# Optimization experiments

Hardware: AMD Instinct MI355X
Metric: run time of the kernel (lower is better)

## Reference

```python
import jax, jax.numpy as jnp
import numpy as np

N = 100000      # nodes
E = 3200000     # edges (before self-loops)
IN = 1          # input feature dim
H1, C = 4, 8    # layer1: 4 heads x 8 channels; layer2: 1 head x 8 channels
NEG_SLOPE = 0.2


def setup_inputs() -> dict:
    key = jax.random.key(0)
    ks = jax.random.split(key, 10)
    x = jax.random.normal(ks[0], (N, IN), jnp.float32)
    edge_index = jax.random.randint(ks[1], (2, E), 0, N, dtype=jnp.int32)
    # layer 1 params (GATConv(1, 8, heads=4))
    W1 = jax.random.normal(ks[2], (IN, H1 * C), jnp.float32) * 0.5
    a_src1 = jax.random.normal(ks[3], (H1, C), jnp.float32) * 0.5
    a_dst1 = jax.random.normal(ks[4], (H1, C), jnp.float32) * 0.5
    b1 = jnp.zeros((H1 * C,), jnp.float32)
    # layer 2 params (GATConv(32, 8, heads=1))
    W2 = jax.random.normal(ks[5], (H1 * C, C), jnp.float32) * 0.2
    a_src2 = jax.random.normal(ks[6], (1, C), jnp.float32) * 0.5
    a_dst2 = jax.random.normal(ks[7], (1, C), jnp.float32) * 0.5
    b2 = jnp.zeros((C,), jnp.float32)
    return {"x": x, "edge_index": edge_index, "W1": W1, "a_src1": a_src1,
            "a_dst1": a_dst1, "b1": b1, "W2": W2, "a_src2": a_src2,
            "a_dst2": a_dst2, "b2": b2}


def _gat_layer(x, src, dst, W, a_s, a_d, b, heads, ch):
    # Linear transform per head: [N, heads, ch]
    h = (x @ W).reshape(-1, heads, ch)
    # per-node attention logits
    al_s = jnp.einsum('nhc,hc->nh', h, a_s)  # [N, H]
    al_d = jnp.einsum('nhc,hc->nh', h, a_d)  # [N, H]
    # per-edge logits (message src -> dst)
    e = jax.nn.leaky_relu(al_s[src] + al_d[dst], NEG_SLOPE)  # [E', H]
    # segment softmax over incoming edges of each dst node
    m = jax.ops.segment_max(e, dst, num_segments=N)          # [N, H]
    e = jnp.exp(e - m[dst])
    s = jax.ops.segment_sum(e, dst, num_segments=N)          # [N, H]
    alpha = e / s[dst]                                       # [E', H]
    # weighted scatter-add aggregation
    out = jax.ops.segment_sum(h[src] * alpha[:, :, None], dst, num_segments=N)
    return out.reshape(N, heads * ch) + b


def reference(x, edge_index, W1, a_src1, a_dst1, b1, W2, a_src2, a_dst2, b2):
    loops = jnp.arange(N, dtype=edge_index.dtype)
    src = jnp.concatenate([edge_index[0], loops])  # add self-loops (PyG default)
    dst = jnp.concatenate([edge_index[1], loops])
    h = _gat_layer(x, src, dst, W1, a_src1, a_dst1, b1, H1, C)
    h = jax.nn.relu(h)
    out = _gat_layer(h, src, dst, W2, a_src2, a_dst2, b2, 1, C)
    return out
```

## Files before the change

kernel.cpp:

```cpp
#include <hip/hip_runtime.h>
#include <hip/hip_bf16.h>

#define NEG_SLOPE 0.2f


__global__ void prep_consts(const float* __restrict__ W1,
                            const float* __restrict__ as1,
                            const float* __restrict__ ad1,
                            float* __restrict__ consts) {
    int t = threadIdx.x;
    if (t >= 8) return;
    int h = t & 3;
    const float* a = (t < 4) ? as1 : ad1;
    float s = 0.f;
    #pragma unroll
    for (int c = 0; c < 8; ++c)
        s += W1[h * 8 + c] * a[h * 8 + c];
    consts[t] = s;
}

__global__ void bucket_hist(const int* __restrict__ ei, int* __restrict__ gcnt, int E) {
    __shared__ int cnt[2048];
    int t = threadIdx.x;
    for (int i = t; i < 2048; i += 256) cnt[i] = 0;
    __syncthreads();
    int stride = gridDim.x * 256;
    for (int e = blockIdx.x * 256 + t; e < E; e += stride)
        atomicAdd(&cnt[ei[E + e] >> 6], 1);
    __syncthreads();
    for (int i = t; i < 2048; i += 256) {
        int c = cnt[i];
        if (c) atomicAdd(&gcnt[i], c);
    }
}

__global__ void scan_init(const int* __restrict__ gcnt,
                          int* __restrict__ gbase, int* __restrict__ gcursor) {
    __shared__ int buf[512];
    int t = threadIdx.x;
    int c0 = gcnt[t * 4], c1 = gcnt[t * 4 + 1], c2 = gcnt[t * 4 + 2], c3 = gcnt[t * 4 + 3];
    int sum = c0 + c1 + c2 + c3;
    buf[t] = sum;
    __syncthreads();
    for (int o = 1; o < 512; o <<= 1) {
        int add = (t >= o) ? buf[t - o] : 0;
        __syncthreads();
        buf[t] += add;
        __syncthreads();
    }
    int base = buf[t] - sum;
    gbase[t * 4] = base;     gcursor[t * 4] = base;     base += c0;
    gbase[t * 4 + 1] = base; gcursor[t * 4 + 1] = base; base += c1;
    gbase[t * 4 + 2] = base; gcursor[t * 4 + 2] = base; base += c2;
    gbase[t * 4 + 3] = base; gcursor[t * 4 + 3] = base;
}

__global__ void bucket_scatter(const int* __restrict__ ei, int* __restrict__ gcursor,
                               unsigned int* __restrict__ pairs, int E) {
    __shared__ int cnt[2048];
    __shared__ int basel[2048];
    int t = threadIdx.x;
    int chunk = (E + gridDim.x - 1) / gridDim.x;
    int lo = blockIdx.x * chunk;
    int hi = min(E, lo + chunk);
    for (int i = t; i < 2048; i += 1024) cnt[i] = 0;
    __syncthreads();
    for (int e = lo + t; e < hi; e += 1024)
        atomicAdd(&cnt[ei[E + e] >> 6], 1);
    __syncthreads();
    for (int i = t; i < 2048; i += 1024) {
        int c = cnt[i];
        basel[i] = c ? atomicAdd(&gcursor[i], c) : 0;
        cnt[i] = 0;
    }
    __syncthreads();
    for (int e = lo + t; e < hi; e += 1024) {
        int s = ei[e];
        int d = ei[E + e];
        int bk = d >> 6;
        int loc = atomicAdd(&cnt[bk], 1);
        pairs[basel[bk] + loc] = (unsigned)s | ((unsigned)(d & 63) << 17);
    }
}

__global__ void l1_comb(const float* __restrict__ x,
                        const int* __restrict__ gbase, const int* __restrict__ gcnt,
                        const unsigned int* __restrict__ pairs,
                        const float* __restrict__ consts,
                        const float* __restrict__ W1, const float* __restrict__ b1,
                        const float* __restrict__ W2,
                        const float* __restrict__ as2, const float* __restrict__ ad2,
                        float* __restrict__ h2, float* __restrict__ als2,
                        float* __restrict__ ald2, int N) {
    __shared__ __align__(16) float R[4 * 64 * 8];
    __shared__ float xl[64];
    int t = threadIdx.x;
    int lane = t & 63;
    int bk = blockIdx.x;
    int node0 = bk << 6;
    int nw = min(64, N - node0);
    for (int i = t; i < 4 * 64 * 8; i += 256) R[i] = 0.f;
    if (t < nw) xl[t] = x[node0 + t];
    float S[4], D[4];
    #pragma unroll
    for (int h = 0; h < 4; ++h) { S[h] = consts[h]; D[h] = consts[4 + h]; }
    __syncthreads();
    float* wreg = &R[(t >> 6) * 512];
    int b = gbase[bk];
    int hi = b + gcnt[bk];
    for (int i = b + t; i < hi; i += 256) {
        unsigned p = pairs[i];
        int src = (int)(p & 131071u);
        int ld  = (int)(p >> 17);
        float xs = x[src];
        float xd = xl[ld];
        float w[4];
        #pragma unroll
        for (int h = 0; h < 4; ++h) {
            float v = xs * S[h] + xd * D[h];
            v = (v > 0.f) ? v : NEG_SLOPE * v;
            w[h] = __expf(v);
        }
        unsigned long long mask = ~0ull;
        #pragma unroll
        for (int bit = 0; bit < 6; ++bit) {
            unsigned long long bb = __ballot((ld >> bit) & 1);
            mask &= ((ld >> bit) & 1) ? bb : ~bb;
        }
        mask &= __ballot(1);
        int rank = __popcll(mask & ((1ull << lane) - 1ull));
        float* row = &wreg[ld * 8];
        for (int r = 0; r < 64; ++r) {
            if (__ballot(rank == r) == 0ull) break;
            if (rank == r) {
                row[0] += w[0]; row[1] += w[1]; row[2] += w[2]; row[3] += w[3];
                row[4] = fmaf(w[0], xs, row[4]); row[5] = fmaf(w[1], xs, row[5]);
                row[6] = fmaf(w[2], xs, row[6]); row[7] = fmaf(w[3], xs, row[7]);
            }
        }
    }
    __syncthreads();
    if (t < nw) {
        int n = node0 + t;
        float xn = xl[t];
        float o[8];
        #pragma unroll
        for (int c = 0; c < 8; ++c) o[c] = 0.f;
        #pragma unroll
        for (int h = 0; h < 4; ++h) {
            float v = xn * (S[h] + D[h]);
            v = (v > 0.f) ? v : NEG_SLOPE * v;
            float ww = __expf(v);
            float s1 = R[t * 8 + h] + R[512 + t * 8 + h]
                     + R[1024 + t * 8 + h] + R[1536 + t * 8 + h] + ww;
            float t1 = R[t * 8 + 4 + h] + R[512 + t * 8 + 4 + h]
                     + R[1024 + t * 8 + 4 + h] + R[1536 + t * 8 + 4 + h] + ww * xn;
            float tt = t1 / s1;
            #pragma unroll
            for (int c = 0; c < 8; ++c) {
                float r = fmaxf(tt * W1[h * 8 + c] + b1[h * 8 + c], 0.f);
                #pragma unroll
                for (int c2 = 0; c2 < 8; ++c2) o[c2] += r * W2[(h * 8 + c) * 8 + c2];
            }
        }
        float as = 0.f, ad = 0.f;
        #pragma unroll
        for (int c = 0; c < 8; ++c) { as += o[c] * as2[c]; ad += o[c] * ad2[c]; }
        float4* hv = (float4*)&h2[(size_t)n * 8];
        hv[0] = make_float4(o[0], o[1], o[2], o[3]);
        hv[1] = make_float4(o[4], o[5], o[6], o[7]);
        als2[n] = as;
        ald2[n] = ad;
    }
}

__global__ void l2_comb(const int* __restrict__ gbase, const int* __restrict__ gcnt,
                        const unsigned int* __restrict__ pairs,
                        const float* __restrict__ als2, const float* __restrict__ ald2,
                        const float* __restrict__ h2, const float* __restrict__ b2,
                        float* __restrict__ out, int N) {
    __shared__ __align__(16) float R[4 * 64 * 12];
    __shared__ float adl[64];
    int t = threadIdx.x;
    int lane = t & 63;
    int bk = blockIdx.x;
    int node0 = bk << 6;
    int nw = min(64, N - node0);
    for (int i = t; i < 4 * 64 * 12; i += 256) R[i] = 0.f;
    if (t < nw) adl[t] = ald2[node0 + t];
    __syncthreads();
    float* wreg = &R[(t >> 6) * 768];
    int b = gbase[bk];
    int hi = b + gcnt[bk];
    for (int i = b + t; i < hi; i += 256) {
        unsigned p = pairs[i];
        int src = (int)(p & 131071u);
        int ld  = (int)(p >> 17);
        float a = als2[src];
        const float4* hv = (const float4*)&h2[(size_t)src * 8];
        float4 ha = hv[0], hb = hv[1];
        float v = a + adl[ld];
        v = (v > 0.f) ? v : NEG_SLOPE * v;
        float w = __expf(v);
        unsigned long long mask = ~0ull;
        #pragma unroll
        for (int bit = 0; bit < 6; ++bit) {
            unsigned long long bb = __ballot((ld >> bit) & 1);
            mask &= ((ld >> bit) & 1) ? bb : ~bb;
        }
        mask &= __ballot(1);
        int rank = __popcll(mask & ((1ull << lane) - 1ull));
        float* row = &wreg[ld * 12];
        for (int r = 0; r < 64; ++r) {
            if (__ballot(rank == r) == 0ull) break;
            if (rank == r) {
                row[0] += w;
                row[1] = fmaf(w, ha.x, row[1]); row[2] = fmaf(w, ha.y, row[2]);
                row[3] = fmaf(w, ha.z, row[3]); row[4] = fmaf(w, ha.w, row[4]);
                row[5] = fmaf(w, hb.x, row[5]); row[6] = fmaf(w, hb.y, row[6]);
                row[7] = fmaf(w, hb.z, row[7]); row[8] = fmaf(w, hb.w, row[8]);
            }
        }
    }
    __syncthreads();
    if (t < nw) {
        int n = node0 + t;
        float v = als2[n] + adl[t];
        v = (v > 0.f) ? v : NEG_SLOPE * v;
        float ww = __expf(v);
        const float4* hv = (const float4*)&h2[(size_t)n * 8];
        float4 ha0 = hv[0], hb0 = hv[1];
        float acc[9];
        #pragma unroll
        for (int c = 0; c < 9; ++c)
            acc[c] = R[t * 12 + c] + R[768 + t * 12 + c]
                   + R[1536 + t * 12 + c] + R[2304 + t * 12 + c];
        float s2 = acc[0] + ww;
        float inv = 1.f / s2;
        float4* ov = (float4*)&out[(size_t)n * 8];
        ov[0] = make_float4((acc[1] + ww * ha0.x) * inv + b2[0],
                            (acc[2] + ww * ha0.y) * inv + b2[1],
                            (acc[3] + ww * ha0.z) * inv + b2[2],
                            (acc[4] + ww * ha0.w) * inv + b2[3]);
        ov[1] = make_float4((acc[5] + ww * hb0.x) * inv + b2[4],
                            (acc[6] + ww * hb0.y) * inv + b2[5],
                            (acc[7] + ww * hb0.z) * inv + b2[6],
                            (acc[8] + ww * hb0.w) * inv + b2[7]);
    }
}


__global__ void edge_pass1(const int* __restrict__ ei, const float* __restrict__ x,
                           const float* __restrict__ consts,
                           float* __restrict__ s1, float* __restrict__ t1, int E, int N) {
    int e = blockIdx.x * blockDim.x + threadIdx.x;
    if (e >= E + N) return;
    int src, dst;
    if (e < E) { src = ei[e]; dst = ei[E + e]; }
    else       { src = dst = e - E; }
    float xs = x[src], xd = x[dst];
    #pragma unroll
    for (int h = 0; h < 4; ++h) {
        float v = xs * consts[h] + xd * consts[4 + h];
        v = (v > 0.f) ? v : NEG_SLOPE * v;
        float w = __expf(v);
        atomicAdd(&s1[dst * 4 + h], w);
        atomicAdd(&t1[dst * 4 + h], w * xs);
    }
}

__global__ void node_mid(const float* __restrict__ s1, const float* __restrict__ t1,
                         const float* __restrict__ W1, const float* __restrict__ b1,
                         const float* __restrict__ W2,
                         const float* __restrict__ as2, const float* __restrict__ ad2,
                         float* __restrict__ h2, float* __restrict__ als2,
                         float* __restrict__ ald2, int N) {
    int n = blockIdx.x * blockDim.x + threadIdx.x;
    if (n >= N) return;
    float o[8];
    #pragma unroll
    for (int c = 0; c < 8; ++c) o[c] = 0.f;
    #pragma unroll
    for (int h = 0; h < 4; ++h) {
        float t = t1[n * 4 + h] / s1[n * 4 + h];
        #pragma unroll
        for (int c = 0; c < 8; ++c) {
            float r = fmaxf(t * W1[h * 8 + c] + b1[h * 8 + c], 0.f);
            #pragma unroll
            for (int c2 = 0; c2 < 8; ++c2) o[c2] += r * W2[(h * 8 + c) * 8 + c2];
        }
    }
    float as = 0.f, ad = 0.f;
    #pragma unroll
    for (int c = 0; c < 8; ++c) { h2[n * 8 + c] = o[c]; as += o[c] * as2[c]; ad += o[c] * ad2[c]; }
    als2[n] = as; ald2[n] = ad;
}

__global__ void edge_pass2(const int* __restrict__ ei, const float* __restrict__ als2,
                           const float* __restrict__ ald2, const float* __restrict__ h2,
                           float* __restrict__ s2, float* __restrict__ acc2, int E, int N) {
    int e = blockIdx.x * blockDim.x + threadIdx.x;
    if (e >= E + N) return;
    int src, dst;
    if (e < E) { src = ei[e]; dst = ei[E + e]; }
    else       { src = dst = e - E; }
    float v = als2[src] + ald2[dst];
    v = (v > 0.f) ? v : NEG_SLOPE * v;
    float w = __expf(v);
    atomicAdd(&s2[dst], w);
    const float4* hs = (const float4*)&h2[src * 8];
    float4 a = hs[0], bq = hs[1];
    float* acc = &acc2[dst * 8];
    atomicAdd(&acc[0], w * a.x);  atomicAdd(&acc[1], w * a.y);
    atomicAdd(&acc[2], w * a.z);  atomicAdd(&acc[3], w * a.w);
    atomicAdd(&acc[4], w * bq.x); atomicAdd(&acc[5], w * bq.y);
    atomicAdd(&acc[6], w * bq.z); atomicAdd(&acc[7], w * bq.w);
}

__global__ void node_out(const float* __restrict__ s2, const float* __restrict__ acc2,
                         const float* __restrict__ b2, float* __restrict__ out, int N) {
    int i = blockIdx.x * blockDim.x + threadIdx.x;
    if (i >= N * 8) return;
    out[i] = acc2[i] / s2[i >> 3] + b2[i & 7];
}


extern "C" void kernel_launch(void* const* d_in, const int* in_sizes, int n_in,
                              void* d_out, int out_size, void* d_ws, size_t ws_size,
                              hipStream_t stream) {
    const float* x   = (const float*)d_in[0];
    const int*   ei  = (const int*)d_in[1];
    const float* W1  = (const float*)d_in[2];
    const float* as1 = (const float*)d_in[3];
    const float* ad1 = (const float*)d_in[4];
    const float* b1  = (const float*)d_in[5];
    const float* W2  = (const float*)d_in[6];
    const float* as2 = (const float*)d_in[7];
    const float* ad2 = (const float*)d_in[8];
    const float* b2  = (const float*)d_in[9];
    float* out = (float*)d_out;

    const int N = in_sizes[0];
    const int E = in_sizes[1] / 2;
    const int NBK = (N + 63) >> 6;

    float* ws = (float*)d_ws;
    size_t need = (size_t)(16 + 3 * 2048 + 10 * (size_t)N + (size_t)E) * sizeof(float);

    if (N <= 131072 && ws_size >= need) {
        float*    consts  = ws;
        int*      gcnt    = (int*)(ws + 16);
        int*      gbase   = gcnt + 2048;
        int*      gcursor = gbase + 2048;
        float*    als2    = ws + 16 + 3 * 2048;
        float*    ald2    = als2 + N;
        float*    h2      = ald2 + N;
        unsigned* pairs   = (unsigned*)(h2 + 8 * (size_t)N);

        hipMemsetAsync(gcnt, 0, 2048 * sizeof(int), stream);
        prep_consts<<<1, 64, 0, stream>>>(W1, as1, ad1, consts);
        bucket_hist<<<128, 256, 0, stream>>>(ei, gcnt, E);
        scan_init<<<1, 512, 0, stream>>>(gcnt, gbase, gcursor);
        bucket_scatter<<<256, 1024, 0, stream>>>(ei, gcursor, pairs, E);
        l1_comb<<<NBK, 256, 0, stream>>>(x, gbase, gcnt, pairs, consts,
                                         W1, b1, W2, as2, ad2, h2, als2, ald2, N);
        l2_comb<<<NBK, 256, 0, stream>>>(gbase, gcnt, pairs, als2, ald2, h2, b2, out, N);
    } else {
        float* consts = ws;
        float* s1   = ws + 16;
        float* t1   = s1 + 4 * (size_t)N;
        float* h2   = t1 + 4 * (size_t)N;
        float* als2 = h2 + 8 * (size_t)N;
        float* ald2 = als2 + (size_t)N;
        float* s2   = ald2 + (size_t)N;
        float* acc2 = s2 + (size_t)N;

        hipMemsetAsync(ws, 0, (16 + 8 * (size_t)N) * sizeof(float), stream);
        hipMemsetAsync(s2, 0, 9 * (size_t)N * sizeof(float), stream);
        prep_consts<<<1, 64, 0, stream>>>(W1, as1, ad1, consts);
        int total = E + N;
        edge_pass1<<<(total + 255) / 256, 256, 0, stream>>>(ei, x, consts, s1, t1, E, N);
        node_mid<<<(N + 255) / 256, 256, 0, stream>>>(s1, t1, W1, b1, W2, as2, ad2, h2, als2, ald2, N);
        edge_pass2<<<(total + 255) / 256, 256, 0, stream>>>(ei, als2, ald2, h2, s2, acc2, E, N);
        node_out<<<(N * 8 + 255) / 256, 256, 0, stream>>>(s2, acc2, b2, out, N);
    }
}
```

Measured before the change: 223.8 us.

## Vectorize edge-index loads, fuse const prep, widen comb kernels with prefetch

Bucket histogram and scatter kernels now read destination and source indices as int4 vectors, with scalar head and tail loops for unaligned ends. The per-head constant computation is folded into the scan kernel, removing one launch. The l1/l2 combine kernels move from 256 to 512 threads with eight shared-memory partial-sum regions, and software-prefetch the next packed edge. The intent is to cut load instruction count and launch overhead and raise memory-level parallelism, at the cost of doubled shared memory per block and more reduction work in the epilogue.

```diff
diff --git a/kernel.cpp b/kernel.cpp
--- a/kernel.cpp
+++ b/kernel.cpp
@@ -4,29 +4,28 @@
 #define NEG_SLOPE 0.2f
 
 
-__global__ void prep_consts(const float* __restrict__ W1,
-                            const float* __restrict__ as1,
-                            const float* __restrict__ ad1,
-                            float* __restrict__ consts) {
-    int t = threadIdx.x;
-    if (t >= 8) return;
-    int h = t & 3;
-    const float* a = (t < 4) ? as1 : ad1;
-    float s = 0.f;
-    #pragma unroll
-    for (int c = 0; c < 8; ++c)
-        s += W1[h * 8 + c] * a[h * 8 + c];
-    consts[t] = s;
-}
-
 __global__ void bucket_hist(const int* __restrict__ ei, int* __restrict__ gcnt, int E) {
     __shared__ int cnt[2048];
     int t = threadIdx.x;
     for (int i = t; i < 2048; i += 256) cnt[i] = 0;
     __syncthreads();
-    int stride = gridDim.x * 256;
-    for (int e = blockIdx.x * 256 + t; e < E; e += stride)
-        atomicAdd(&cnt[ei[E + e] >> 6], 1);
+    const int* dei = ei + E;
+    int gid = blockIdx.x * 256 + t;
+    int gstride = gridDim.x * 256;
+    if ((E & 3) == 0) {
+        const int4* dei4 = (const int4*)dei;
+        int E4 = E >> 2;
+        for (int v = gid; v < E4; v += gstride) {
+            int4 d = dei4[v];
+            atomicAdd(&cnt[d.x >> 6], 1);
+            atomicAdd(&cnt[d.y >> 6], 1);
+            atomicAdd(&cnt[d.z >> 6], 1);
+            atomicAdd(&cnt[d.w >> 6], 1);
+        }
+    } else {
+        for (int e = gid; e < E; e += gstride)
+            atomicAdd(&cnt[dei[e] >> 6], 1);
+    }
     __syncthreads();
     for (int i = t; i < 2048; i += 256) {
         int c = cnt[i];
@@ -35,9 +34,22 @@
 }
 
 __global__ void scan_init(const int* __restrict__ gcnt,
-                          int* __restrict__ gbase, int* __restrict__ gcursor) {
+                          int* __restrict__ gbase, int* __restrict__ gcursor,
+                          const float* __restrict__ W1,
+                          const float* __restrict__ as1,
+                          const float* __restrict__ ad1,
+                          float* __restrict__ consts) {
     __shared__ int buf[512];
     int t = threadIdx.x;
+    if (t < 8) {
+        int h = t & 3;
+        const float* a = (t < 4) ? as1 : ad1;
+        float s = 0.f;
+        #pragma unroll
+        for (int c = 0; c < 8; ++c)
+            s += W1[h * 8 + c] * a[h * 8 + c];
+        consts[t] = s;
+    }
     int c0 = gcnt[t * 4], c1 = gcnt[t * 4 + 1], c2 = gcnt[t * 4 + 2], c3 = gcnt[t * 4 + 3];
     int sum = c0 + c1 + c2 + c3;
     buf[t] = sum;
@@ -63,10 +75,29 @@
     int chunk = (E + gridDim.x - 1) / gridDim.x;
     int lo = blockIdx.x * chunk;
     int hi = min(E, lo + chunk);
+    const int* dei = ei + E;
     for (int i = t; i < 2048; i += 1024) cnt[i] = 0;
     __syncthreads();
-    for (int e = lo + t; e < hi; e += 1024)
-        atomicAdd(&cnt[ei[E + e] >> 6], 1);
+    bool vec = ((E & 3) == 0);
+    int lo4 = (lo + 3) & ~3;
+    int end4 = hi & ~3;
+    if (vec && end4 > lo4) {
+        for (int e = lo + t; e < lo4; e += 1024)
+            atomicAdd(&cnt[dei[e] >> 6], 1);
+        const int4* dei4 = (const int4*)dei;
+        for (int v = (lo4 >> 2) + t; v < (end4 >> 2); v += 1024) {
+            int4 d = dei4[v];
+            atomicAdd(&cnt[d.x >> 6], 1);
+            atomicAdd(&cnt[d.y >> 6], 1);
+            atomicAdd(&cnt[d.z >> 6], 1);
+            atomicAdd(&cnt[d.w >> 6], 1);
+        }
+        for (int e = end4 + t; e < hi; e += 1024)
+            atomicAdd(&cnt[dei[e] >> 6], 1);
+    } else {
+        for (int e = lo + t; e < hi; e += 1024)
+            atomicAdd(&cnt[dei[e] >> 6], 1);
+    }
     __syncthreads();
     for (int i = t; i < 2048; i += 1024) {
         int c = cnt[i];
@@ -74,12 +105,41 @@
         cnt[i] = 0;
     }
     __syncthreads();
-    for (int e = lo + t; e < hi; e += 1024) {
-        int s = ei[e];
-        int d = ei[E + e];
-        int bk = d >> 6;
-        int loc = atomicAdd(&cnt[bk], 1);
-        pairs[basel[bk] + loc] = (unsigned)s | ((unsigned)(d & 63) << 17);
+    if (vec && end4 > lo4) {
+        for (int e = lo + t; e < lo4; e += 1024) {
+            int s = ei[e], d = dei[e];
+            int bk = d >> 6;
+            int loc = atomicAdd(&cnt[bk], 1);
+            pairs[basel[bk] + loc] = (unsigned)s | ((unsigned)(d & 63) << 17);
+        }
+        const int4* sei4 = (const int4*)ei;
+        const int4* dei4 = (const int4*)dei;
+        for (int v = (lo4 >> 2) + t; v < (end4 >> 2); v += 1024) {
+            int4 sv = sei4[v];
+            int4 dv = dei4[v];
+            int bk0 = dv.x >> 6, bk1 = dv.y >> 6, bk2 = dv.z >> 6, bk3 = dv.w >> 6;
+            int l0 = atomicAdd(&cnt[bk0], 1);
+            pairs[basel[bk0] + l0] = (unsigned)sv.x | ((unsigned)(dv.x & 63) << 17);
+            int l1 = atomicAdd(&cnt[bk1], 1);
+            pairs[basel[bk1] + l1] = (unsigned)sv.y | ((unsigned)(dv.y & 63) << 17);
+            int l2 = atomicAdd(&cnt[bk2], 1);
+            pairs[basel[bk2] + l2] = (unsigned)sv.z | ((unsigned)(dv.z & 63) << 17);
+            int l3 = atomicAdd(&cnt[bk3], 1);
+            pairs[basel[bk3] + l3] = (unsigned)sv.w | ((unsigned)(dv.w & 63) << 17);
+        }
+        for (int e = end4 + t; e < hi; e += 1024) {
+            int s = ei[e], d = dei[e];
+            int bk = d >> 6;
+            int loc = atomicAdd(&cnt[bk], 1);
+            pairs[basel[bk] + loc] = (unsigned)s | ((unsigned)(d & 63) << 17);
+        }
+    } else {
+        for (int e = lo + t; e < hi; e += 1024) {
+            int s = ei[e], d = dei[e];
+            int bk = d >> 6;
+            int loc = atomicAdd(&cnt[bk], 1);
+            pairs[basel[bk] + loc] = (unsigned)s | ((unsigned)(d & 63) << 17);
+        }
     }
 }
 
@@ -92,14 +152,14 @@
                         const float* __restrict__ as2, const float* __restrict__ ad2,
                         float* __restrict__ h2, float* __restrict__ als2,
                         float* __restrict__ ald2, int N) {
-    __shared__ __align__(16) float R[4 * 64 * 8];
+    __shared__ __align__(16) float R[8 * 64 * 8];
     __shared__ float xl[64];
     int t = threadIdx.x;
     int lane = t & 63;
     int bk = blockIdx.x;
     int node0 = bk << 6;
     int nw = min(64, N - node0);
-    for (int i = t; i < 4 * 64 * 8; i += 256) R[i] = 0.f;
+    for (int i = t; i < 8 * 64 * 8; i += 512) R[i] = 0.f;
     if (t < nw) xl[t] = x[node0 + t];
     float S[4], D[4];
     #pragma unroll
@@ -108,8 +168,12 @@
     float* wreg = &R[(t >> 6) * 512];
     int b = gbase[bk];
     int hi = b + gcnt[bk];
-    for (int i = b + t; i < hi; i += 256) {
-        unsigned p = pairs[i];
+    int i = b + t;
+    unsigned p = (i < hi) ? pairs[i] : 0u;
+    while (i < hi) {
+        int inx = i + 512;
+        unsigned pn = 0u;
+        if (inx < hi) pn = pairs[inx];
         int src = (int)(p & 131071u);
         int ld  = (int)(p >> 17);
         float xs = x[src];
@@ -138,6 +202,7 @@
                 row[6] = fmaf(w[2], xs, row[6]); row[7] = fmaf(w[3], xs, row[7]);
             }
         }
+        p = pn; i = inx;
     }
     __syncthreads();
     if (t < nw) {
@@ -151,16 +216,18 @@
             float v = xn * (S[h] + D[h]);
             v = (v > 0.f) ? v : NEG_SLOPE * v;
             float ww = __expf(v);
-            float s1 = R[t * 8 + h] + R[512 + t * 8 + h]
-                     + R[1024 + t * 8 + h] + R[1536 + t * 8 + h] + ww;
-            float t1 = R[t * 8 + 4 + h] + R[512 + t * 8 + 4 + h]
-                     + R[1024 + t * 8 + 4 + h] + R[1536 + t * 8 + 4 + h] + ww * xn;
+            float s1 = ww, t1 = ww * xn;
+            #pragma unroll
+            for (int r = 0; r < 8; ++r) {
+                s1 += R[r * 512 + t * 8 + h];
+                t1 += R[r * 512 + t * 8 + 4 + h];
+            }
             float tt = t1 / s1;
             #pragma unroll
             for (int c = 0; c < 8; ++c) {
-                float r = fmaxf(tt * W1[h * 8 + c] + b1[h * 8 + c], 0.f);
+                float rr = fmaxf(tt * W1[h * 8 + c] + b1[h * 8 + c], 0.f);
                 #pragma unroll
-                for (int c2 = 0; c2 < 8; ++c2) o[c2] += r * W2[(h * 8 + c) * 8 + c2];
+                for (int c2 = 0; c2 < 8; ++c2) o[c2] += rr * W2[(h * 8 + c) * 8 + c2];
             }
         }
         float as = 0.f, ad = 0.f;
@@ -179,21 +246,25 @@
                         const float* __restrict__ als2, const float* __restrict__ ald2,
                         const float* __restrict__ h2, const float* __restrict__ b2,
                         float* __restrict__ out, int N) {
-    __shared__ __align__(16) float R[4 * 64 * 12];
+    __shared__ __align__(16) float R[8 * 64 * 12];
     __shared__ float adl[64];
     int t = threadIdx.x;
     int lane = t & 63;
     int bk = blockIdx.x;
     int node0 = bk << 6;
     int nw = min(64, N - node0);
-    for (int i = t; i < 4 * 64 * 12; i += 256) R[i] = 0.f;
+    for (int i = t; i < 8 * 64 * 12; i += 512) R[i] = 0.f;
     if (t < nw) adl[t] = ald2[node0 + t];
     __syncthreads();
     float* wreg = &R[(t >> 6) * 768];
     int b = gbase[bk];
     int hi = b + gcnt[bk];
-    for (int i = b + t; i < hi; i += 256) {
-        unsigned p = pairs[i];
+    int i = b + t;
+    unsigned p = (i < hi) ? pairs[i] : 0u;
+    while (i < hi) {
+        int inx = i + 512;
+        unsigned pn = 0u;
+        if (inx < hi) pn = pairs[inx];
         int src = (int)(p & 131071u);
         int ld  = (int)(p >> 17);
         float a = als2[src];
@@ -221,6 +292,7 @@
                 row[7] = fmaf(w, hb.z, row[7]); row[8] = fmaf(w, hb.w, row[8]);
             }
         }
+        p = pn; i = inx;
     }
     __syncthreads();
     if (t < nw) {
@@ -232,9 +304,12 @@
         float4 ha0 = hv[0], hb0 = hv[1];
         float acc[9];
         #pragma unroll
-        for (int c = 0; c < 9; ++c)
-            acc[c] = R[t * 12 + c] + R[768 + t * 12 + c]
-                   + R[1536 + t * 12 + c] + R[2304 + t * 12 + c];
+        for (int c = 0; c < 9; ++c) {
+            float s = 0.f;
+            #pragma unroll
+            for (int r = 0; r < 8; ++r) s += R[r * 768 + t * 12 + c];
+            acc[c] = s;
+        }
         float s2 = acc[0] + ww;
         float inv = 1.f / s2;
         float4* ov = (float4*)&out[(size_t)n * 8];
@@ -249,6 +324,21 @@
     }
 }
 
+
+__global__ void prep_consts(const float* __restrict__ W1,
+                            const float* __restrict__ as1,
+                            const float* __restrict__ ad1,
+                            float* __restrict__ consts) {
+    int t = threadIdx.x;
+    if (t >= 8) return;
+    int h = t & 3;
+    const float* a = (t < 4) ? as1 : ad1;
+    float s = 0.f;
+    #pragma unroll
+    for (int c = 0; c < 8; ++c)
+        s += W1[h * 8 + c] * a[h * 8 + c];
+    consts[t] = s;
+}
 
 __global__ void edge_pass1(const int* __restrict__ ei, const float* __restrict__ x,
                            const float* __restrict__ consts,
@@ -358,13 +448,12 @@
         unsigned* pairs   = (unsigned*)(h2 + 8 * (size_t)N);
 
         hipMemsetAsync(gcnt, 0, 2048 * sizeof(int), stream);
-        prep_consts<<<1, 64, 0, stream>>>(W1, as1, ad1, consts);
-        bucket_hist<<<128, 256, 0, stream>>>(ei, gcnt, E);
-        scan_init<<<1, 512, 0, stream>>>(gcnt, gbase, gcursor);
+        bucket_hist<<<256, 256, 0, stream>>>(ei, gcnt, E);
+        scan_init<<<1, 512, 0, stream>>>(gcnt, gbase, gcursor, W1, as1, ad1, consts);
         bucket_scatter<<<256, 1024, 0, stream>>>(ei, gcursor, pairs, E);
-        l1_comb<<<NBK, 256, 0, stream>>>(x, gbase, gcnt, pairs, consts,
+        l1_comb<<<NBK, 512, 0, stream>>>(x, gbase, gcnt, pairs, consts,
                                          W1, b1, W2, as2, ad2, h2, als2, ald2, N);
-        l2_comb<<<NBK, 256, 0, stream>>>(gbase, gcnt, pairs, als2, ald2, h2, b2, out, N);
+        l2_comb<<<NBK, 512, 0, stream>>>(gbase, gcnt, pairs, als2, ald2, h2, b2, out, N);
     } else {
         float* consts = ws;
         float* s1   = ws + 16;
```

New measurement: 200.6 us. -10.4%, faster.
